# Kernel tuning notes

Measured on AMD Instinct MI355X. Metric: run time of the kernel, lower is better.

The kernel has to match this reference:

```python
import jax, jax.numpy as jnp
import numpy as np

N_NODES = 100000
D = 128
N_EDGES = 800000


def setup_inputs() -> dict:
    key = jax.random.key(0)
    k_feat, k_src, k_dst, k_ws, k_wn = jax.random.split(key, 5)
    scale = 1.0 / np.sqrt(D)
    return {
        "features": jax.random.normal(k_feat, (N_NODES, D), jnp.float32),
        "src": jax.random.randint(k_src, (N_EDGES,), 0, N_NODES, jnp.int32),
        "dst": jax.random.randint(k_dst, (N_EDGES,), 0, N_NODES, jnp.int32),
        "gamma": jnp.ones((D,), jnp.float32),
        "beta": jnp.zeros((D,), jnp.float32),
        "W_self": jax.random.normal(k_ws, (D, D), jnp.float32) * scale,
        "W_neigh": jax.random.normal(k_wn, (D, D), jnp.float32) * scale,
        "b": jnp.zeros((D,), jnp.float32),
    }


def reference(features, src, dst, gamma, beta, W_self, W_neigh, b):
    n = features.shape[0]
    eps = 1e-5
    # BatchNorm1d (training mode: batch stats over the node dim, biased var)
    mean = jnp.mean(features, axis=0)
    var = jnp.mean(jnp.square(features - mean), axis=0)
    h = (features - mean) * jax.lax.rsqrt(var + eps) * gamma + beta  # [N, D]

    # SAGEConv 'mean': gather source feats along edges, mean-reduce per dst node
    msg = h[src]  # [E, D] irregular gather
    agg = jax.ops.segment_sum(msg, dst, num_segments=n)  # [N, D]
    deg = jax.ops.segment_sum(jnp.ones(src.shape, h.dtype), dst, num_segments=n)
    h_neigh = agg / jnp.maximum(deg, 1.0)[:, None]  # zero-degree nodes stay 0

    conv = h @ W_self + h_neigh @ W_neigh + b  # fc_self + fc_neigh + bias
    out = conv + h  # skip connection
    return jax.nn.gelu(out, approximate=False)
```

## Files before the change

### kernel.cpp

```cpp
#include <hip/hip_runtime.h>

#define DD 128
#define NPB_LOG 8
#define NPB 256
#define EPB 2048

typedef __attribute__((ext_vector_type(8))) short short8;
typedef __attribute__((ext_vector_type(4))) float f32x4;
typedef __attribute__((ext_vector_type(2))) float f32x2;

__device__ inline unsigned short f2bf(float f) {
    unsigned u = __float_as_uint(f);
    unsigned r = u + 0x7fffu + ((u >> 16) & 1u);
    return (unsigned short)(r >> 16);
}

__global__ __launch_bounds__(256) void phase1_k(
    const float4* __restrict__ x, float* __restrict__ stats16, int n,
    const int* __restrict__ dst, int nE, int NCHUNK, int NBUCK,
    const float* __restrict__ Wself, const float* __restrict__ Wneigh,
    unsigned short* __restrict__ Bpre, int* __restrict__ cm) {
    int b = blockIdx.x, tid = threadIdx.x;
    __shared__ float ls[8][256];
    if (b < NCHUNK) {
        int chunk = b;
        int* cnt = (int*)ls;
        for (int i = tid; i < NBUCK; i += 256) cnt[i] = 0;
        __syncthreads();
        int e0 = chunk * EPB;
#pragma unroll
        for (int j = 0; j < 8; ++j) {
            int e = e0 + j * 256 + tid;
            if (e < nE) atomicAdd(&cnt[dst[e] >> NPB_LOG], 1);
        }
        __syncthreads();
        for (int bk = tid; bk < NBUCK; bk += 256)
            cm[(size_t)bk * NCHUNK + chunk] = cnt[bk];
    } else if (b < NCHUNK + 16) {
        int q = (b - NCHUNK) * 256 + tid;
        int l = q & 63;
        int kb = ((q >> 9) << 5) + ((l >> 4) << 3);
        int nn = (((q >> 6) & 7) << 4) + (l & 15);
        bool self = (kb < 128);
        const float* Wp = self ? (Wself + (size_t)kb * 128 + nn)
                               : (Wneigh + (size_t)(kb - 128) * 128 + nn);
        unsigned tmp[4];
#pragma unroll
        for (int j = 0; j < 4; ++j) {
            float v0 = Wp[(2 * j) * 128];
            float v1 = Wp[(2 * j + 1) * 128];
            if (self) {
                if (kb + 2 * j == nn) v0 += 1.0f;
                if (kb + 2 * j + 1 == nn) v1 += 1.0f;
            }
            tmp[j] = (unsigned)f2bf(v0) | ((unsigned)f2bf(v1) << 16);
        }
        uint4 w; w.x = tmp[0]; w.y = tmp[1]; w.z = tmp[2]; w.w = tmp[3];
        *(uint4*)(Bpre + (size_t)q * 8) = w;
    } else {
        int bb = b - NCHUNK - 16;
        int c4 = tid & 31, sub = tid >> 5;
        float sx = 0.f, sy = 0.f, sz = 0.f, sw = 0.f;
        float qx = 0.f, qy = 0.f, qz = 0.f, qw = 0.f;
        for (int r = bb * 8 + sub; r < n; r += 1024 * 8) {
            float4 v = x[(size_t)r * 32 + c4];
            sx += v.x; sy += v.y; sz += v.z; sw += v.w;
            qx += v.x * v.x; qy += v.y * v.y; qz += v.z * v.z; qw += v.w * v.w;
        }
        ls[sub][c4 * 4 + 0] = sx; ls[sub][c4 * 4 + 1] = sy;
        ls[sub][c4 * 4 + 2] = sz; ls[sub][c4 * 4 + 3] = sw;
        ls[sub][128 + c4 * 4 + 0] = qx; ls[sub][128 + c4 * 4 + 1] = qy;
        ls[sub][128 + c4 * 4 + 2] = qz; ls[sub][128 + c4 * 4 + 3] = qw;
        __syncthreads();
        float t = 0.f;
#pragma unroll
        for (int k = 0; k < 8; ++k) t += ls[k][tid];
        atomicAdd(&stats16[(bb & 15) * 256 + tid], t);
    }
}

__global__ __launch_bounds__(256) void scanA_k(
    const int* __restrict__ v_in, int* __restrict__ bsum, int n) {
    int b = blockIdx.x, t = threadIdx.x;
    int i0 = b * 1024 + t * 4;
    int4 v = {0, 0, 0, 0};
    if (i0 + 3 < n) v = *(const int4*)(v_in + i0);
    else {
        if (i0 < n) v.x = v_in[i0];
        if (i0 + 1 < n) v.y = v_in[i0 + 1];
        if (i0 + 2 < n) v.z = v_in[i0 + 2];
    }
    __shared__ int ls[256];
    ls[t] = v.x + v.y + v.z + v.w;
    __syncthreads();
#pragma unroll
    for (int off = 128; off > 0; off >>= 1) {
        if (t < off) ls[t] += ls[t + off];
        __syncthreads();
    }
    if (t == 0) bsum[b] = ls[0];
}

__global__ __launch_bounds__(256) void scanB_k(
    const int* __restrict__ bsum, int* __restrict__ bpref,
    int* __restrict__ total_out, int nb, int n,
    const float* __restrict__ stats16, const float* __restrict__ gamma,
    const float* __restrict__ beta, float* __restrict__ scsh, float inv_n) {
    int t = threadIdx.x;
    if (t < 128) {
        float s = 0.f, q = 0.f;
#pragma unroll
        for (int sh = 0; sh < 16; ++sh) {
            s += stats16[sh * 256 + t];
            q += stats16[sh * 256 + 128 + t];
        }
        float mean = s * inv_n;
        float var = q * inv_n - mean * mean;
        float sc = rsqrtf(var + 1e-5f) * gamma[t];
        scsh[t] = sc;
        scsh[128 + t] = beta[t] - mean * sc;
    }
    __shared__ int ls[256];
    ls[t] = (t < nb) ? bsum[t] : 0;
    __syncthreads();
#pragma unroll
    for (int off = 1; off < 256; off <<= 1) {
        int x = (t >= off) ? ls[t - off] : 0;
        __syncthreads();
        ls[t] += x;
        __syncthreads();
    }
    if (t < nb) bpref[t] = (t == 0) ? 0 : ls[t - 1];
    if (t == nb - 1) total_out[n] = ls[t];
}

__global__ __launch_bounds__(256) void scanC_k(
    const int* __restrict__ v_in, const int* __restrict__ bpref,
    int* __restrict__ o1, int* __restrict__ o2, int n) {
    int b = blockIdx.x, t = threadIdx.x;
    int i0 = b * 1024 + t * 4;
    int4 v = {0, 0, 0, 0};
    if (i0 + 3 < n) v = *(const int4*)(v_in + i0);
    else {
        if (i0 < n) v.x = v_in[i0];
        if (i0 + 1 < n) v.y = v_in[i0 + 1];
        if (i0 + 2 < n) v.z = v_in[i0 + 2];
    }
    int s = v.x + v.y + v.z + v.w;
    __shared__ int ls[256];
    ls[t] = s;
    __syncthreads();
#pragma unroll
    for (int off = 1; off < 256; off <<= 1) {
        int x = (t >= off) ? ls[t - off] : 0;
        __syncthreads();
        ls[t] += x;
        __syncthreads();
    }
    int run = bpref[b] + ((t == 0) ? 0 : ls[t - 1]);
    int4 o;
    o.x = run; o.y = run + v.x; o.z = o.y + v.y; o.w = o.z + v.z;
    if (i0 + 3 < n) {
        *(int4*)(o1 + i0) = o;
        *(int4*)(o2 + i0) = o;
    } else {
        if (i0 < n) { o1[i0] = o.x; o2[i0] = o.x; }
        if (i0 + 1 < n) { o1[i0 + 1] = o.y; o2[i0 + 1] = o.y; }
        if (i0 + 2 < n) { o1[i0 + 2] = o.z; o2[i0 + 2] = o.z; }
    }
}

__global__ __launch_bounds__(256) void phase2_k(
    const float4* __restrict__ x, const float* __restrict__ scsh,
    uint2* __restrict__ hbuf, unsigned* __restrict__ h8, int n,
    const int* __restrict__ src, const int* __restrict__ dst,
    const int* __restrict__ cmscan, unsigned* __restrict__ pairs,
    int nE, int NCHUNK, int NBUCK) {
    int b = blockIdx.x, tid = threadIdx.x;
    __shared__ int shr[512];
    if (b < NCHUNK) {
        int chunk = b;
        for (int i = tid; i < NBUCK; i += 256)
            shr[i] = cmscan[(size_t)i * NCHUNK + chunk];
        __syncthreads();
        int e0 = chunk * EPB;
#pragma unroll
        for (int j = 0; j < 8; ++j) {
            int e = e0 + j * 256 + tid;
            if (e < nE) {
                int d = dst[e];
                int p = atomicAdd(&shr[d >> NPB_LOG], 1);
                pairs[p] = ((unsigned)src[e] << NPB_LOG) | (unsigned)(d & (NPB - 1));
            }
        }
    } else {
        int blk = b - NCHUNK;
        int c4 = tid & 31, sub = tid >> 5;
        int r0 = blk * 16 + sub, r1 = r0 + 8;
        float4 sc = ((const float4*)scsh)[c4];
        float4 sh = ((const float4*)(scsh + 128))[c4];
        bool ok0 = r0 < n, ok1 = r1 < n;
        float4 v0, v1;
        if (ok0) v0 = x[(size_t)r0 * 32 + c4];
        if (ok1) v1 = x[(size_t)r1 * 32 + c4];
        if (ok0) {
            float hx = v0.x * sc.x + sh.x, hy = v0.y * sc.y + sh.y;
            float hz = v0.z * sc.z + sh.z, hw = v0.w * sc.w + sh.w;
            uint2 o;
            o.x = (unsigned)f2bf(hx) | ((unsigned)f2bf(hy) << 16);
            o.y = (unsigned)f2bf(hz) | ((unsigned)f2bf(hw) << 16);
            hbuf[(size_t)r0 * 32 + c4] = o;
            int p8 = __builtin_amdgcn_cvt_pk_fp8_f32(hx, hy, 0, false);
            p8 = __builtin_amdgcn_cvt_pk_fp8_f32(hz, hw, p8, true);
            h8[(size_t)r0 * 32 + c4] = (unsigned)p8;
        }
        if (ok1) {
            float hx = v1.x * sc.x + sh.x, hy = v1.y * sc.y + sh.y;
            float hz = v1.z * sc.z + sh.z, hw = v1.w * sc.w + sh.w;
            uint2 o;
            o.x = (unsigned)f2bf(hx) | ((unsigned)f2bf(hy) << 16);
            o.y = (unsigned)f2bf(hz) | ((unsigned)f2bf(hw) << 16);
            hbuf[(size_t)r1 * 32 + c4] = o;
            int p8 = __builtin_amdgcn_cvt_pk_fp8_f32(hx, hy, 0, false);
            p8 = __builtin_amdgcn_cvt_pk_fp8_f32(hz, hw, p8, true);
            h8[(size_t)r1 * 32 + c4] = (unsigned)p8;
        }
    }
}

__global__ __launch_bounds__(256) void sortC_k(
    const unsigned* __restrict__ pairs, const int* __restrict__ cmscan,
    int* __restrict__ offsets, int* __restrict__ csr,
    int n, int nE, int NCHUNK, int NBUCK) {
    int b = blockIdx.x, tid = threadIdx.x;
    int base0 = cmscan[(size_t)b * NCHUNK];
    int end = (b + 1 < NBUCK) ? cmscan[(size_t)(b + 1) * NCHUNK] : nE;
    __shared__ int cnt[NPB];
    __shared__ int cur[NPB];
    cnt[tid] = 0;
    __syncthreads();
    for (int e = base0 + tid; e < end; e += 256)
        atomicAdd(&cnt[pairs[e] & (NPB - 1)], 1);
    __syncthreads();
    int c0 = cnt[tid];
    __shared__ int ps[256];
    ps[tid] = c0;
    __syncthreads();
#pragma unroll
    for (int off = 1; off < 256; off <<= 1) {
        int v = (tid >= off) ? ps[tid - off] : 0;
        __syncthreads();
        ps[tid] += v;
        __syncthreads();
    }
    int ex = base0 + ps[tid] - c0;
    cur[tid] = ex;
    int node = b * NPB + tid;
    if (node < n) offsets[node] = ex;
    if (b == NBUCK - 1 && tid == 0) offsets[n] = nE;
    __syncthreads();
    for (int e = base0 + tid; e < end; e += 256) {
        unsigned u = pairs[e];
        int p = atomicAdd(&cur[u & (NPB - 1)], 1);
        csr[p] = (int)(u >> NPB_LOG);
    }
}

#define ACC8(v)                                                       \
    do {                                                              \
        acc[0] += __builtin_amdgcn_cvt_pk_f32_fp8((v).x, false);      \
        acc[1] += __builtin_amdgcn_cvt_pk_f32_fp8((v).x, true);       \
        acc[2] += __builtin_amdgcn_cvt_pk_f32_fp8((v).y, false);      \
        acc[3] += __builtin_amdgcn_cvt_pk_f32_fp8((v).y, true);       \
        acc[4] += __builtin_amdgcn_cvt_pk_f32_fp8((v).z, false);      \
        acc[5] += __builtin_amdgcn_cvt_pk_f32_fp8((v).z, true);       \
        acc[6] += __builtin_amdgcn_cvt_pk_f32_fp8((v).w, false);      \
        acc[7] += __builtin_amdgcn_cvt_pk_f32_fp8((v).w, true);       \
    } while (0)

__global__ __launch_bounds__(256) void pull_k(
    const int* __restrict__ offsets, const int* __restrict__ csr,
    const uint4* __restrict__ h8q, uint4* __restrict__ hnw, int n) {
    int wv = (blockIdx.x * 256 + threadIdx.x) >> 6;
    int lane = threadIdx.x & 63;
    int g = lane >> 3, sl = lane & 7;
    int node = wv * 8 + g;
    bool valid = node < n;
    int nc = valid ? node : (n - 1);
    int b0 = offsets[nc], b1 = offsets[nc + 1];
    f32x2 acc[8];
#pragma unroll
    for (int k = 0; k < 8; ++k) acc[k] = f32x2{0.f, 0.f};
    int j = b0;
    for (; j + 4 <= b1; j += 4) {
        int i0 = csr[j], i1 = csr[j + 1], i2 = csr[j + 2], i3 = csr[j + 3];
        uint4 v0 = h8q[(size_t)i0 * 8 + sl];
        uint4 v1 = h8q[(size_t)i1 * 8 + sl];
        uint4 v2 = h8q[(size_t)i2 * 8 + sl];
        uint4 v3 = h8q[(size_t)i3 * 8 + sl];
        ACC8(v0); ACC8(v1); ACC8(v2); ACC8(v3);
    }
    if (j + 2 <= b1) {
        int i0 = csr[j], i1 = csr[j + 1];
        uint4 v0 = h8q[(size_t)i0 * 8 + sl];
        uint4 v1 = h8q[(size_t)i1 * 8 + sl];
        ACC8(v0); ACC8(v1);
        j += 2;
    }
    if (j < b1) {
        int i0 = csr[j];
        uint4 v0 = h8q[(size_t)i0 * 8 + sl];
        ACC8(v0);
    }
    if (valid) {
        float rd = (b1 > b0) ? 1.0f / (float)(b1 - b0) : 0.0f;
        unsigned ow[8];
#pragma unroll
        for (int k = 0; k < 8; ++k)
            ow[k] = (unsigned)f2bf(acc[k].x * rd) |
                    ((unsigned)f2bf(acc[k].y * rd) << 16);
        uint4 o1; o1.x = ow[0]; o1.y = ow[1]; o1.z = ow[2]; o1.w = ow[3];
        uint4 o2; o2.x = ow[4]; o2.y = ow[5]; o2.z = ow[6]; o2.w = ow[7];
        hnw[(size_t)node * 16 + sl * 2] = o1;
        hnw[(size_t)node * 16 + sl * 2 + 1] = o2;
    }
}

__global__ __launch_bounds__(256, 2) void gemm_k(
    const unsigned short* __restrict__ h, const unsigned short* __restrict__ hn,
    const unsigned short* __restrict__ Bpre, const float* __restrict__ bias,
    float* __restrict__ out, int n) {
    __shared__ unsigned short Bsw[32768];
    int tid = threadIdx.x, wave = tid >> 6, lane = tid & 63;
    int rb = blockIdx.x;
#pragma unroll
    for (int i = 0; i < 16; ++i) {
        int g = wave * 16 + i;
        __builtin_amdgcn_global_load_lds(
            (const __attribute__((address_space(1))) void*)(
                Bpre + ((size_t)g * 64 + lane) * 8),
            (__attribute__((address_space(3))) void*)(Bsw + (size_t)g * 512),
            16, 0, 0);
    }
    __syncthreads();

    int quad = lane >> 4, mrow = lane & 15;
    int r0 = rb * 128 + wave * 32;
    int rA0 = min(r0 + mrow, n - 1);
    int rA1 = min(r0 + 16 + mrow, n - 1);

    f32x4 zero = {0.0f, 0.0f, 0.0f, 0.0f};
    f32x4 acc[2][8];
#pragma unroll
    for (int m = 0; m < 2; ++m)
#pragma unroll
        for (int t = 0; t < 8; ++t) acc[m][t] = zero;

#pragma unroll
    for (int s = 0; s < 8; ++s) {
        int kb = s * 32 + quad * 8;
        short8 a0, a1;
        if (s < 4) {
            a0 = *(const short8*)(h + (size_t)rA0 * 128 + kb);
            a1 = *(const short8*)(h + (size_t)rA1 * 128 + kb);
        } else {
            int kk = kb - 128;
            a0 = *(const short8*)(hn + (size_t)rA0 * 128 + kk);
            a1 = *(const short8*)(hn + (size_t)rA1 * 128 + kk);
        }
#pragma unroll
        for (int tt = 0; tt < 8; ++tt) {
            short8 b = *(const short8*)(Bsw + ((size_t)(s * 8 + tt) * 64 + lane) * 8);
            acc[0][tt] = __builtin_amdgcn_mfma_f32_16x16x32_bf16(a0, b, acc[0][tt], 0, 0, 0);
            acc[1][tt] = __builtin_amdgcn_mfma_f32_16x16x32_bf16(a1, b, acc[1][tt], 0, 0, 0);
        }
    }

    float bi[8];
#pragma unroll
    for (int t = 0; t < 8; ++t) bi[t] = bias[t * 16 + mrow];
#pragma unroll
    for (int m = 0; m < 2; ++m) {
#pragma unroll
        for (int i = 0; i < 4; ++i) {
            int row = r0 + m * 16 + quad * 4 + i;
            if (row < n) {
#pragma unroll
                for (int t = 0; t < 8; ++t) {
                    int col = t * 16 + mrow;
                    float xv = acc[m][t][i] + bi[t];
                    float x2 = xv * xv;
                    float u = 0.7978845608f * xv * (1.0f + 0.044715f * x2);
                    float e = __expf(2.0f * u);
                    float th = 1.0f - 2.0f * __builtin_amdgcn_rcpf(e + 1.0f);
                    out[(size_t)row * 128 + col] = 0.5f * xv * (1.0f + th);
                }
            }
        }
    }
}

extern "C" void kernel_launch(void* const* d_in, const int* in_sizes, int n_in,
                              void* d_out, int out_size, void* d_ws, size_t ws_size,
                              hipStream_t stream) {
    const float* features = (const float*)d_in[0];
    const int* src = (const int*)d_in[1];
    const int* dst = (const int*)d_in[2];
    const float* gamma = (const float*)d_in[3];
    const float* beta = (const float*)d_in[4];
    const float* Wself = (const float*)d_in[5];
    const float* Wneigh = (const float*)d_in[6];
    const float* bias = (const float*)d_in[7];
    int n = in_sizes[0] / DD;
    int nE = in_sizes[1];
    int NCHUNK = (nE + EPB - 1) / EPB;
    int NBUCK = (n + NPB - 1) / NPB;
    int CM = NBUCK * NCHUNK;
    int tilesCM = (CM + 1023) / 1024;
    int nbNorm16 = (n + 15) / 16;

    auto align1k = [](size_t x) { return (x + 1023) & ~(size_t)1023; };
    char* ws = (char*)d_ws;
    size_t off = 0;
    float* stats16 = (float*)(ws + off);       off += 16384;
    float* scsh   = (float*)(ws + off);        off += 2048;
    int* cm       = (int*)(ws + off);          off += align1k((size_t)(CM + 1) * 4);
    int* cmscan   = (int*)(ws + off);          off += align1k((size_t)CM * 4);
    int* offsets  = (int*)(ws + off);          off += align1k((size_t)(n + 1) * 4);
    int* csr      = (int*)(ws + off);          off += align1k((size_t)nE * 4);
    unsigned* pairs = (unsigned*)(ws + off);   off += align1k((size_t)nE * 4);
    int* bsum     = (int*)(ws + off);          off += 1024;
    int* bpref    = (int*)(ws + off);          off += 1024;
    unsigned short* Bpre = (unsigned short*)(ws + off); off += 65536;
    unsigned short* hbuf = (unsigned short*)(ws + off); off += (size_t)n * 256;
    unsigned short* hnbuf = (unsigned short*)(ws + off); off += (size_t)n * 256;
    unsigned* h8 = (unsigned*)(ws + off);      off += (size_t)n * 128;

    hipMemsetAsync(stats16, 0, 16384, stream);

    phase1_k<<<NCHUNK + 16 + 1024, 256, 0, stream>>>(
        (const float4*)features, stats16, n, dst, nE, NCHUNK, NBUCK,
        Wself, Wneigh, Bpre, cm);
    scanA_k<<<tilesCM, 256, 0, stream>>>(cm, bsum, CM);
    scanB_k<<<1, 256, 0, stream>>>(bsum, bpref, cm, tilesCM, CM,
                                   stats16, gamma, beta, scsh, 1.0f / (float)n);
    scanC_k<<<tilesCM, 256, 0, stream>>>(cm, bpref, cmscan, cmscan, CM);
    phase2_k<<<NCHUNK + nbNorm16, 256, 0, stream>>>(
        (const float4*)features, scsh, (uint2*)hbuf, h8, n,
        src, dst, cmscan, pairs, nE, NCHUNK, NBUCK);
    sortC_k<<<NBUCK, 256, 0, stream>>>(pairs, cmscan, offsets, csr, n, nE,
                                       NCHUNK, NBUCK);
    {
        int waves = (n + 7) / 8;
        int blocks = (waves * 64 + 255) / 256;
        pull_k<<<blocks, 256, 0, stream>>>(
            offsets, csr, (const uint4*)h8, (uint4*)hnbuf, n);
    }
    gemm_k<<<(n + 127) / 128, 256, 0, stream>>>(
        hbuf, hnbuf, Bpre, bias, (float*)d_out, n);
}
```

Before: 196.5 us.

## Locally sort edge chunk by bucket in LDS before scattering pairs

The edge-binning part of phase2 now counts bucket sizes per chunk, runs a Blelloch scan in shared memory, sorts the chunk's pairs into LDS by bucket, and then writes them out contiguously. The aim is to turn random scattered global writes into mostly coalesced runs per bucket. In exchange it adds several barriers, a scan, extra LDS use (about 16KB) that may lower occupancy, and a second pass over the dst values.

```diff
diff --git a/kernel.cpp b/kernel.cpp
--- a/kernel.cpp
+++ b/kernel.cpp
@@ -177,21 +177,57 @@
     const int* __restrict__ cmscan, unsigned* __restrict__ pairs,
     int nE, int NCHUNK, int NBUCK) {
     int b = blockIdx.x, tid = threadIdx.x;
-    __shared__ int shr[512];
+    __shared__ int a[512];
+    __shared__ int lcur[512];
+    __shared__ int bas[512];
+    __shared__ unsigned lsorted[EPB];
+    __shared__ unsigned short lbk[EPB];
     if (b < NCHUNK) {
         int chunk = b;
-        for (int i = tid; i < NBUCK; i += 256)
-            shr[i] = cmscan[(size_t)i * NCHUNK + chunk];
-        __syncthreads();
         int e0 = chunk * EPB;
+        int nv = min(EPB, nE - e0);
+        for (int i = tid; i < 512; i += 256) a[i] = 0;
+        __syncthreads();
+        int myd[8];
 #pragma unroll
         for (int j = 0; j < 8; ++j) {
             int e = e0 + j * 256 + tid;
-            if (e < nE) {
-                int d = dst[e];
-                int p = atomicAdd(&shr[d >> NPB_LOG], 1);
-                pairs[p] = ((unsigned)src[e] << NPB_LOG) | (unsigned)(d & (NPB - 1));
+            int d = (e < nE) ? dst[e] : -1;
+            myd[j] = d;
+            if (d >= 0) atomicAdd(&a[d >> NPB_LOG], 1);
+        }
+        for (int bk = tid; bk < NBUCK; bk += 256)
+            bas[bk] = cmscan[(size_t)bk * NCHUNK + chunk];
+        __syncthreads();
+        for (int d = 1; d < 512; d <<= 1) {
+            int idx = (tid + 1) * (d << 1) - 1;
+            if (idx < 512) a[idx] += a[idx - d];
+            __syncthreads();
+        }
+        if (tid == 0) a[511] = 0;
+        __syncthreads();
+        for (int d = 256; d >= 1; d >>= 1) {
+            int idx = (tid + 1) * (d << 1) - 1;
+            if (idx < 512) { int tm = a[idx - d]; a[idx - d] = a[idx]; a[idx] += tm; }
+            __syncthreads();
+        }
+        for (int i = tid; i < 512; i += 256) lcur[i] = a[i];
+        __syncthreads();
+#pragma unroll
+        for (int j = 0; j < 8; ++j) {
+            int d = myd[j];
+            if (d >= 0) {
+                int e = e0 + j * 256 + tid;
+                int bk = d >> NPB_LOG;
+                int lp = atomicAdd(&lcur[bk], 1);
+                lsorted[lp] = ((unsigned)src[e] << NPB_LOG) | (unsigned)(d & (NPB - 1));
+                lbk[lp] = (unsigned short)bk;
             }
+        }
+        __syncthreads();
+        for (int i = tid; i < nv; i += 256) {
+            int bk = lbk[i];
+            pairs[bas[bk] + i - a[bk]] = lsorted[i];
         }
     } else {
         int blk = b - NCHUNK;
```

After: 192.4 us. -2.1%, faster.
